# Kernel optimization log

Hardware: AMD Instinct MI355X
Metric: run time of the kernel (lower is better)

The kernel has to match this reference:

```python
import jax, jax.numpy as jnp
import numpy as np
from jax import lax

B, C_IN, C_OUT, K, W_DIM, H, W = 16, 512, 512, 3, 512, 64, 64


def setup_inputs() -> dict:
    key = jax.random.key(0)
    k1, k2, k3, k4, k5 = jax.random.split(key, 5)
    fan_in = C_IN * K * K
    bound = 1.0 / np.sqrt(fan_in)
    imgs = jax.random.normal(k1, (B, C_IN, H, W), dtype=jnp.float32)
    w_embs = jax.random.normal(k2, (B, W_DIM), dtype=jnp.float32)
    conv_weight = jax.random.uniform(k3, (C_OUT, C_IN, K, K), jnp.float32, -bound, bound)
    conv_bias = jax.random.uniform(k4, (C_OUT,), jnp.float32, -bound, bound)
    sb = 1.0 / np.sqrt(W_DIM)
    style_W = jax.random.uniform(k5, (C_IN, W_DIM), jnp.float32, -sb, sb)
    style_b = jnp.zeros((C_IN,), jnp.float32)
    return {"imgs": imgs, "w_embs": w_embs, "conv_weight": conv_weight,
            "conv_bias": conv_bias, "style_W": style_W, "style_b": style_b}


def reference(imgs, w_embs, conv_weight, conv_bias, style_W, style_b):
    b, c, h, w = imgs.shape
    out_dim, in_dim, ky, kx = conv_weight.shape
    # style modulation: (b, in_dim), +1 as in the torch module
    style = w_embs @ style_W.T + style_b + 1.0
    # per-sample weights: (b, out_dim, in_dim, ky, kx)
    weight = conv_weight[None] * style[:, None, :, None, None]
    # demodulation: exact L2 norm over (in_dim, ky, kx) (no eps, matching torch)
    norm = jnp.sqrt(jnp.sum(weight * weight, axis=(2, 3, 4), keepdims=True))
    weight = weight / norm
    # grouped conv with groups = batch
    x = imgs.reshape(1, b * c, h, w)
    k = weight.reshape(b * out_dim, in_dim, ky, kx)
    y = lax.conv_general_dilated(
        x, k, window_strides=(1, 1), padding="SAME",
        feature_group_count=b,
        dimension_numbers=("NCHW", "OIHW", "NCHW"))
    y = y.reshape(b, out_dim, h, w)
    return y + conv_bias[None, :, None, None]
```

## Files before the change

### kernel.cpp

```cpp
#include <hip/hip_runtime.h>


typedef __bf16 bf16x8 __attribute__((ext_vector_type(8)));
typedef float f32x4 __attribute__((ext_vector_type(4)));

__device__ __forceinline__ void async16(const void* g, void* s) {
  __builtin_amdgcn_global_load_lds((const __attribute__((address_space(1))) void*)g,
                                   (__attribute__((address_space(3))) void*)s, 16, 0, 0);
}

__global__ __launch_bounds__(256) void k_style(const float* __restrict__ we,
                                               const float* __restrict__ sW,
                                               const float* __restrict__ sb,
                                               float* __restrict__ style) {
  int lane = threadIdx.x & 63, wid = threadIdx.x >> 6;
  int b = blockIdx.x >> 7;
  int i = ((blockIdx.x & 127) << 2) + wid;
  const float* wer = we + b * 512;
  const float* swr = sW + i * 512;
  float acc = 0.f;
  for (int d = lane; d < 512; d += 64) acc += wer[d] * swr[d];
#pragma unroll
  for (int off = 32; off; off >>= 1) acc += __shfl_xor(acc, off);
  if (lane == 0) style[b * 512 + i] = acc + sb[i] + 1.0f;
}

__global__ __launch_bounds__(256) void k_wsq(const float* __restrict__ cw,
                                             float* __restrict__ wsq) {
  int t = blockIdx.x * 256 + threadIdx.x;
  const float* p = cw + (long)t * 9;
  float s = 0.f;
#pragma unroll
  for (int k = 0; k < 9; ++k) s += p[k] * p[k];
  wsq[t] = s;
}

__global__ __launch_bounds__(256) void k_rnorm(const float* __restrict__ style,
                                               const float* __restrict__ wsq,
                                               float* __restrict__ rnorm) {
  int lane = threadIdx.x & 63, wid = threadIdx.x >> 6;
  int idx = blockIdx.x * 4 + wid;
  int b = idx >> 9, o = idx & 511;
  float acc = 0.f;
  for (int i = lane; i < 512; i += 64) {
    float s = style[(b << 9) + i];
    acc += s * s * wsq[(o << 9) + i];
  }
#pragma unroll
  for (int off = 32; off; off >>= 1) acc += __shfl_xor(acc, off);
  if (lane == 0) rnorm[idx] = rsqrtf(acc);
}

__global__ __launch_bounds__(256) void k_wt(const float* __restrict__ cw,
                                            const float* __restrict__ style,
                                            const float* __restrict__ rnorm,
                                            __bf16* __restrict__ wt) {
  int t = blockIdx.x * 256 + threadIdx.x;
  int b = t >> 18;
  int oi = t & 262143;
  int o = oi >> 9, i = oi & 511;
  float sc = style[(b << 9) + i] * rnorm[(b << 9) + o];
  const float* p = cw + (long)oi * 9;
#pragma unroll
  for (int k = 0; k < 9; ++k) {
    int tp = (k % 3) * 3 + k / 3;
    wt[((long)(b * 9 + tp) << 18) + ((long)o << 9) + i] = (__bf16)(p[k] * sc);
  }
}

__global__ __launch_bounds__(256) void k_xpad(const float* __restrict__ imgs,
                                              __bf16* __restrict__ xpad) {
  int t = blockIdx.x * 256 + threadIdx.x;
  if (t >= 16 * 4356) return;
  int b = t / 4356;
  int rc = t - b * 4356;
  int r = rc / 66, c = rc - (rc / 66) * 66;
  __bf16* dst = xpad + (long)t * 512;
  if (r == 0 || r == 65 || c == 0 || c == 65) {
    const f32x4 z = {0.f, 0.f, 0.f, 0.f};
#pragma unroll 4
    for (int j = 0; j < 64; ++j) *(f32x4*)(dst + j * 8) = z;
  } else {
    const float* src = imgs + ((long)b << 21) + ((r - 1) << 6) + (c - 1);
    for (int j = 0; j < 64; ++j) {
      bf16x8 v;
#pragma unroll
      for (int q = 0; q < 8; ++q) v[q] = (__bf16)src[(long)(j * 8 + q) << 12];
      *(bf16x8*)(dst + j * 8) = v;
    }
  }
}

__global__ __launch_bounds__(256, 3) void k_conv(const __bf16* __restrict__ xpad,
                                                 const __bf16* __restrict__ wt,
                                                 const float* __restrict__ bias,
                                                 float* __restrict__ out) {
  __shared__ __attribute__((aligned(16))) __bf16 sX[224 * 64];
  __shared__ __attribute__((aligned(16))) __bf16 sA3[3 * 128 * 32];

  const int tid = threadIdx.x;
  const int lane = tid & 63;
  const int wid = tid >> 6;
  const int wr = wid >> 1, wc = wid & 1;
  const int l15 = lane & 15, lq = lane >> 4;

  const int bid = blockIdx.x;
  const int b = bid >> 7;
  const int r7 = bid & 127;
  const int o0 = (r7 >> 5) << 7;
  const int st = r7 & 31;
  const int h0 = (st >> 1) << 2;
  const int w0 = (st & 1) << 5;

  const __bf16* xg[7];
#pragma unroll
  for (int it = 0; it < 7; ++it) {
    int s = it * 256 + tid;
    int p = s >> 3;
    int pp = (p < 204) ? p : 0;
    int j = (s & 7) ^ (pp & 7);
    int lr = pp / 34, lc = pp - lr * 34;
    xg[it] = xpad + ((long)((b * 66 + h0 + lr) * 66) + (w0 + lc)) * 512 + j * 8;
  }
  const int abase = ((o0 + (tid >> 2)) << 9) + (((tid & 3) ^ ((tid >> 3) & 3)) << 3);
  const __bf16* wtb = wt + (long)b * 2359296;

  f32x4 acc[4][4];
  const f32x4 zero4 = {0.f, 0.f, 0.f, 0.f};
#pragma unroll
  for (int m = 0; m < 4; ++m)
#pragma unroll
    for (int n = 0; n < 4; ++n) acc[m][n] = zero4;

  const int arowbase = (wr << 6) + l15;
  const int csA = (lq ^ ((l15 >> 1) & 3)) << 3;
  const int rbase = wc << 1;

  bool first = true;
  for (int icb = 0; icb < 8; ++icb) {
    const int ic = icb << 6;
#pragma unroll
    for (int hf = 0; hf < 2; ++hf) {
#pragma unroll
      for (int kx = 0; kx < 3; ++kx) {
        if (!first) __syncthreads();
        first = false;
        if (hf == 0 && kx == 0) {
#pragma unroll
          for (int it = 0; it < 7; ++it)
            async16(xg[it] + ic, (char*)sX + it * 4096 + (wid << 10));
        }
        {
          const __bf16* wa = wtb + abase + ic + (hf << 5);
#pragma unroll
          for (int it = 0; it < 6; ++it)
            async16(wa + (kx * 3 + (it >> 1)) * 262144 + (it & 1) * 32768,
                    (char*)sA3 + it * 4096 + (wid << 10));
        }
        __syncthreads();
        const int jb = (hf << 2) | lq;
        bf16x8 bfr[4][2];
#pragma unroll
        for (int r = 0; r < 4; ++r)
#pragma unroll
          for (int c = 0; c < 2; ++c) {
            int p = (rbase + r) * 34 + (c << 4) + l15 + kx;
            bfr[r][c] = *(const bf16x8*)&sX[(p << 6) + ((jb ^ (p & 7)) << 3)];
          }
#pragma unroll
        for (int ky = 0; ky < 3; ++ky) {
          const __bf16* sAb = sA3 + ky * 4096;
          bf16x8 af[4];
#pragma unroll
          for (int m = 0; m < 4; ++m)
            af[m] = *(const bf16x8*)&sAb[((arowbase + (m << 4)) << 5) + csA];
#pragma unroll
          for (int m = 0; m < 4; ++m)
#pragma unroll
            for (int q = 0; q < 2; ++q)
#pragma unroll
              for (int c = 0; c < 2; ++c)
                acc[m][(q << 1) + c] = __builtin_amdgcn_mfma_f32_16x16x32_bf16(
                    af[m], bfr[q + ky][c], acc[m][(q << 1) + c], 0, 0, 0);
        }
      }
    }
  }

  float* outb = out + ((long)b << 21);
#pragma unroll
  for (int m = 0; m < 4; ++m) {
    int ob = o0 + (wr << 6) + (m << 4) + (lq << 2);
#pragma unroll
    for (int n = 0; n < 4; ++n) {
      int nn = (wc << 6) + (n << 4) + l15;
      int h = h0 + (nn >> 5), w = w0 + (nn & 31);
#pragma unroll
      for (int q = 0; q < 4; ++q) {
        int o = ob + q;
        outb[((long)o << 12) + (h << 6) + w] = acc[m][n][q] + bias[o];
      }
    }
  }
}

extern "C" void kernel_launch(void* const* d_in, const int* in_sizes, int n_in,
                              void* d_out, int out_size, void* d_ws, size_t ws_size,
                              hipStream_t stream) {
  const float* imgs = (const float*)d_in[0];
  const float* w_embs = (const float*)d_in[1];
  const float* cw = (const float*)d_in[2];
  const float* bias = (const float*)d_in[3];
  const float* style_W = (const float*)d_in[4];
  const float* style_b = (const float*)d_in[5];
  float* out = (float*)d_out;

  char* ws = (char*)d_ws;
  float* style = (float*)(ws);
  float* rnorm = (float*)(ws + (32 << 10));
  float* wsq = (float*)(ws + (64 << 10));
  __bf16* wt = (__bf16*)(ws + (64 << 10) + (1 << 20));
  __bf16* xpad = (__bf16*)(ws + (64 << 10) + (1 << 20) + 75497472);
  size_t need = (size_t)(64 << 10) + (1 << 20) + 75497472ull + 71368704ull;
  if (ws_size < need) return;

  k_style<<<2048, 256, 0, stream>>>(w_embs, style_W, style_b, style);
  k_wsq<<<1024, 256, 0, stream>>>(cw, wsq);
  k_rnorm<<<2048, 256, 0, stream>>>(style, wsq, rnorm);
  k_wt<<<16384, 256, 0, stream>>>(cw, style, rnorm, wt);
  k_xpad<<<273, 256, 0, stream>>>(imgs, xpad);
  k_conv<<<2048, 256, 0, stream>>>(xpad, wt, bias, out);
}
```

Baseline: 391.0 us.

## Double conv spatial tile height to 8 rows per block

The conv block now covers 8 output rows by 32 columns instead of 4 by 32, halving the grid to 1024 blocks. Each wave computes 4x8 MFMA tiles, so every loaded weight fragment feeds twice as many MFMAs and the halo overhead per output drops. The cost is more accumulator registers, a larger input tile in LDS (10 rows by 34), and occupancy lowered to 2 blocks per CU, with fewer blocks to cover the device.

```diff
diff --git a/kernel.cpp b/kernel.cpp
--- a/kernel.cpp
+++ b/kernel.cpp
@@ -91,50 +91,51 @@
   }
 }
 
-__global__ __launch_bounds__(256, 3) void k_conv(const __bf16* __restrict__ xpad,
+__global__ __launch_bounds__(256, 2) void k_conv(const __bf16* __restrict__ xpad,
                                                  const __bf16* __restrict__ wt,
                                                  const float* __restrict__ bias,
                                                  float* __restrict__ out) {
-  __shared__ __attribute__((aligned(16))) __bf16 sX[224 * 64];
+  __shared__ __attribute__((aligned(16))) __bf16 sX[2816 * 8];
   __shared__ __attribute__((aligned(16))) __bf16 sA3[3 * 128 * 32];
 
   const int tid = threadIdx.x;
   const int lane = tid & 63;
   const int wid = tid >> 6;
-  const int wr = wid >> 1, wc = wid & 1;
+  const int wr = wid >> 1, wp = wid & 1;
   const int l15 = lane & 15, lq = lane >> 4;
 
   const int bid = blockIdx.x;
-  const int b = bid >> 7;
-  const int r7 = bid & 127;
-  const int o0 = (r7 >> 5) << 7;
-  const int st = r7 & 31;
-  const int h0 = (st >> 1) << 2;
+  const int b = bid >> 6;
+  const int r6 = bid & 63;
+  const int o0 = (r6 >> 4) << 7;
+  const int st = r6 & 15;
+  const int h0 = (st >> 1) << 3;
   const int w0 = (st & 1) << 5;
-
-  const __bf16* xg[7];
-#pragma unroll
-  for (int it = 0; it < 7; ++it) {
+  const int b66 = b * 66;
+
+  const __bf16* xg[11];
+#pragma unroll
+  for (int it = 0; it < 11; ++it) {
     int s = it * 256 + tid;
+    if (s > 2719) s = 2719;
     int p = s >> 3;
-    int pp = (p < 204) ? p : 0;
-    int j = (s & 7) ^ (pp & 7);
-    int lr = pp / 34, lc = pp - lr * 34;
-    xg[it] = xpad + ((long)((b * 66 + h0 + lr) * 66) + (w0 + lc)) * 512 + j * 8;
+    int j = (s & 7) ^ (p & 7);
+    int lr = p / 34, lc = p - (p / 34) * 34;
+    xg[it] = xpad + ((long)((b66 + h0 + lr) * 66) + (w0 + lc)) * 512 + j * 8;
   }
   const int abase = ((o0 + (tid >> 2)) << 9) + (((tid & 3) ^ ((tid >> 3) & 3)) << 3);
   const __bf16* wtb = wt + (long)b * 2359296;
 
-  f32x4 acc[4][4];
+  f32x4 acc[4][8];
   const f32x4 zero4 = {0.f, 0.f, 0.f, 0.f};
 #pragma unroll
   for (int m = 0; m < 4; ++m)
 #pragma unroll
-    for (int n = 0; n < 4; ++n) acc[m][n] = zero4;
+    for (int n = 0; n < 8; ++n) acc[m][n] = zero4;
 
   const int arowbase = (wr << 6) + l15;
   const int csA = (lq ^ ((l15 >> 1) & 3)) << 3;
-  const int rbase = wc << 1;
+  const int rbase = wp << 2;
 
   bool first = true;
   for (int icb = 0; icb < 8; ++icb) {
@@ -147,7 +148,7 @@
         first = false;
         if (hf == 0 && kx == 0) {
 #pragma unroll
-          for (int it = 0; it < 7; ++it)
+          for (int it = 0; it < 11; ++it)
             async16(xg[it] + ic, (char*)sX + it * 4096 + (wid << 10));
         }
         {
@@ -159,9 +160,9 @@
         }
         __syncthreads();
         const int jb = (hf << 2) | lq;
-        bf16x8 bfr[4][2];
-#pragma unroll
-        for (int r = 0; r < 4; ++r)
+        bf16x8 bfr[6][2];
+#pragma unroll
+        for (int r = 0; r < 6; ++r)
 #pragma unroll
           for (int c = 0; c < 2; ++c) {
             int p = (rbase + r) * 34 + (c << 4) + l15 + kx;
@@ -177,11 +178,9 @@
 #pragma unroll
           for (int m = 0; m < 4; ++m)
 #pragma unroll
-            for (int q = 0; q < 2; ++q)
-#pragma unroll
-              for (int c = 0; c < 2; ++c)
-                acc[m][(q << 1) + c] = __builtin_amdgcn_mfma_f32_16x16x32_bf16(
-                    af[m], bfr[q + ky][c], acc[m][(q << 1) + c], 0, 0, 0);
+            for (int n = 0; n < 8; ++n)
+              acc[m][n] = __builtin_amdgcn_mfma_f32_16x16x32_bf16(
+                  af[m], bfr[(n >> 1) + ky][n & 1], acc[m][n], 0, 0, 0);
         }
       }
     }
@@ -192,9 +191,9 @@
   for (int m = 0; m < 4; ++m) {
     int ob = o0 + (wr << 6) + (m << 4) + (lq << 2);
 #pragma unroll
-    for (int n = 0; n < 4; ++n) {
-      int nn = (wc << 6) + (n << 4) + l15;
-      int h = h0 + (nn >> 5), w = w0 + (nn & 31);
+    for (int n = 0; n < 8; ++n) {
+      int pid = (wp << 7) + (n << 4) + l15;
+      int h = h0 + (pid >> 5), w = w0 + (pid & 31);
 #pragma unroll
       for (int q = 0; q < 4; ++q) {
         int o = ob + q;
@@ -229,5 +228,5 @@
   k_rnorm<<<2048, 256, 0, stream>>>(style, wsq, rnorm);
   k_wt<<<16384, 256, 0, stream>>>(cw, style, rnorm, wt);
   k_xpad<<<273, 256, 0, stream>>>(imgs, xpad);
-  k_conv<<<2048, 256, 0, stream>>>(xpad, wt, bias, out);
-}
+  k_conv<<<1024, 256, 0, stream>>>(xpad, wt, bias, out);
+}
```

New measurement: 369.1 us. 1.06x faster.
